# Optimization experiments

Hardware: AMD Instinct MI355X
Metric: run time of the kernel (lower is better)

The kernel has to match this reference:

```python
import jax, jax.numpy as jnp
import numpy as np

D_MODEL = 1024
STATE_DIM = 256


def setup_inputs() -> dict:
    key = jax.random.key(0)
    k_u, k_lam, k_B, k_C = jax.random.split(key, 4)
    u = jax.random.normal(k_u, (4, 4096, D_MODEL), dtype=jnp.float32)
    # log_lambda ~ N(3.0, 0.5^2), matching torch.randn(state_dim)*0.5 + 3.0
    log_lambda = jax.random.normal(k_lam, (STATE_DIM,), dtype=jnp.float32) * 0.5 + 3.0
    # torch Linear weights: B.weight [state_dim, d_model], C.weight [d_model, state_dim]
    B_w = jax.random.normal(k_B, (STATE_DIM, D_MODEL), dtype=jnp.float32) / np.sqrt(D_MODEL)
    C_w = jax.random.normal(k_C, (D_MODEL, STATE_DIM), dtype=jnp.float32) / np.sqrt(STATE_DIM)
    D = jnp.zeros((D_MODEL,), dtype=jnp.float32)
    return {"u": u, "log_lambda": log_lambda, "B_w": B_w, "C_w": C_w, "D": D}


def reference(u, log_lambda, B_w, C_w, D):
    # u: [batch, seq, d_model]
    lam = jax.nn.sigmoid(log_lambda)                      # [state_dim]
    Bu = jnp.einsum('bsd,nd->bsn', u, B_w)                # [batch, seq, state_dim]

    def step(h, bu_t):
        h = lam * h + bu_t                                # [batch, state_dim]
        return h, h

    h0 = jnp.zeros((u.shape[0], lam.shape[0]), dtype=u.dtype)
    # scan over time axis; Bu transposed to [seq, batch, state_dim]
    _, hs = jax.lax.scan(step, h0, jnp.swapaxes(Bu, 0, 1))
    hs = jnp.swapaxes(hs, 0, 1)                           # [batch, seq, state_dim]
    y = jnp.einsum('bsn,dn->bsd', hs, C_w) + D * u        # [batch, seq, d_model]
    return y
```

## Files before the change

kernel.cpp:

```cpp
#include <hip/hip_runtime.h>
#include <math.h>

typedef unsigned short ushort_t;
typedef __bf16 v8bf __attribute__((ext_vector_type(8)));
typedef float f32x4 __attribute__((ext_vector_type(4)));

#define BATCH 4
#define SEQ 4096
#define DM 1024
#define NS 256
#define MROWS (BATCH*SEQ)

#define NCH 128
#define CL (SEQ/NCH)

#define BM 128
#define BN 128
#define BK 32

typedef __attribute__((address_space(1))) void as1_void;
typedef __attribute__((address_space(3))) void as3_void;

__device__ __forceinline__ void gl_lds16(const void* g, void* l) {
    __builtin_amdgcn_global_load_lds((as1_void*)g, (as3_void*)l, 16, 0, 0);
}

__device__ __forceinline__ ushort_t f2bf(float f) {
    unsigned u = __builtin_bit_cast(unsigned, f);
    u += 0x7fff + ((u >> 16) & 1);
    return (ushort_t)(u >> 16);
}

__device__ __forceinline__ float sigm(float x) { return 1.0f / (1.0f + expf(-x)); }

template<bool FUSE_DU>
__global__ __launch_bounds__(256)
void gemm_bt_mfma(const ushort_t* __restrict__ A,
                  const ushort_t* __restrict__ B,
                  float* __restrict__ C,
                  int M, int N, int K,
                  const float* __restrict__ Dvec, const float* __restrict__ U)
{
    __shared__ __align__(16) ushort_t As[BM*BK];
    __shared__ __align__(16) ushort_t Bs[BN*BK];

    const int tid  = threadIdx.x;
    const int lane = tid & 63;
    const int wave = tid >> 6;
    const int wrow = wave >> 1;
    const int wcol = wave & 1;
    const int m0 = blockIdx.x * BM;
    const int n0 = blockIdx.y * BN;

    const int fr = lane & 15;
    const int fq = lane >> 4;

    f32x4 acc[4][4] = {};

    const int ch0 = wave*128 + lane;
    const int ch1 = ch0 + 64;

    for (int k0 = 0; k0 < K; k0 += BK) {
        __syncthreads();
        {
            int r0 = ch0 >> 2, c0 = (ch0 & 3) * 8;
            int r1 = ch1 >> 2, c1 = (ch1 & 3) * 8;
            gl_lds16(&A[(size_t)(m0 + r0)*K + k0 + c0], &As[ch0*8]);
            gl_lds16(&B[(size_t)(n0 + r0)*K + k0 + c0], &Bs[ch0*8]);
            gl_lds16(&A[(size_t)(m0 + r1)*K + k0 + c1], &As[ch1*8]);
            gl_lds16(&B[(size_t)(n0 + r1)*K + k0 + c1], &Bs[ch1*8]);
        }
        __syncthreads();

        v8bf af[4], bf[4];
        #pragma unroll
        for (int mi = 0; mi < 4; ++mi)
            af[mi] = *reinterpret_cast<const v8bf*>(&As[(wrow*64 + mi*16 + fr)*BK + fq*8]);
        #pragma unroll
        for (int ni = 0; ni < 4; ++ni)
            bf[ni] = *reinterpret_cast<const v8bf*>(&Bs[(wcol*64 + ni*16 + fr)*BK + fq*8]);

        #pragma unroll
        for (int mi = 0; mi < 4; ++mi)
            #pragma unroll
            for (int ni = 0; ni < 4; ++ni)
                acc[mi][ni] = __builtin_amdgcn_mfma_f32_16x16x32_bf16(
                                  af[mi], bf[ni], acc[mi][ni], 0, 0, 0);
    }

    const int orow = m0 + wrow*64 + (lane >> 4)*4;
    const int ocol = n0 + wcol*64 + (lane & 15);
    #pragma unroll
    for (int mi = 0; mi < 4; ++mi) {
        #pragma unroll
        for (int ni = 0; ni < 4; ++ni) {
            const int col = ocol + ni*16;
            #pragma unroll
            for (int r = 0; r < 4; ++r) {
                const size_t idx = (size_t)(orow + mi*16 + r) * N + col;
                float v = acc[mi][ni][r];
                if (FUSE_DU) v = fmaf(Dvec[col], U[idx], v);
                C[idx] = v;
            }
        }
    }
}

__global__ __launch_bounds__(256)
void cvt4(const float4* __restrict__ in, ushort_t* __restrict__ out, int n4)
{
    int i = blockIdx.x * 256 + threadIdx.x;
    if (i >= n4) return;
    float4 v = in[i];
    ushort4 o;
    o.x = f2bf(v.x); o.y = f2bf(v.y); o.z = f2bf(v.z); o.w = f2bf(v.w);
    *(ushort4*)&out[4*(size_t)i] = o;
}

__global__ __launch_bounds__(256)
void scan_finals(const float* __restrict__ Bu, const float* __restrict__ ll,
                 float* __restrict__ cf)
{
    const int n = threadIdx.x, c = blockIdx.x, b = blockIdx.y;
    const float lam = sigm(ll[n]);
    const size_t base = ((size_t)b*SEQ + (size_t)c*CL)*NS + n;
    float v[CL];
    #pragma unroll
    for (int t = 0; t < CL; ++t) v[t] = Bu[base + (size_t)t*NS];
    float h = 0.0f;
    #pragma unroll
    for (int t = 0; t < CL; ++t) h = fmaf(lam, h, v[t]);
    cf[((size_t)b*NCH + c)*NS + n] = h;
}

__global__ __launch_bounds__(256)
void carry_scan(const float* __restrict__ ll, const float* __restrict__ cf,
                float* __restrict__ carry)
{
    const int n = threadIdx.x, b = blockIdx.x;
    const float lam = sigm(ll[n]);
    float lamL = lam;
    #pragma unroll
    for (int i = 0; i < 5; ++i) lamL *= lamL;

    const float* cfb = cf    + (size_t)b*NCH*NS + n;
    float*       cab = carry + (size_t)b*NCH*NS + n;

    float x = 0.0f;
    for (int c0 = 0; c0 < NCH; c0 += 16) {
        float v[16];
        #pragma unroll
        for (int j = 0; j < 16; ++j) v[j] = cfb[(size_t)(c0 + j)*NS];
        #pragma unroll
        for (int j = 0; j < 16; ++j) {
            cab[(size_t)(c0 + j)*NS] = x;
            x = fmaf(lamL, x, v[j]);
        }
    }
}

__global__ __launch_bounds__(256)
void scan_apply(const float* __restrict__ Bu, const float* __restrict__ ll,
                const float* __restrict__ carry, ushort_t* __restrict__ hs16)
{
    const int n = threadIdx.x, c = blockIdx.x, b = blockIdx.y;
    const float lam = sigm(ll[n]);
    const size_t base = ((size_t)b*SEQ + (size_t)c*CL)*NS + n;

    float v[CL];
    #pragma unroll
    for (int t = 0; t < CL; ++t) v[t] = Bu[base + (size_t)t*NS];

    float h = carry[((size_t)b*NCH + c)*NS + n];
    #pragma unroll
    for (int t = 0; t < CL; ++t) { h = fmaf(lam, h, v[t]); v[t] = h; }
    #pragma unroll
    for (int t = 0; t < CL; ++t) hs16[base + (size_t)t*NS] = f2bf(v[t]);
}

extern "C" void kernel_launch(void* const* d_in, const int* in_sizes, int n_in,
                              void* d_out, int out_size, void* d_ws, size_t ws_size,
                              hipStream_t stream) {
    const float* u          = (const float*)d_in[0];
    const float* log_lambda = (const float*)d_in[1];
    const float* B_w        = (const float*)d_in[2];
    const float* C_w        = (const float*)d_in[3];
    const float* Dv         = (const float*)d_in[4];
    float* y  = (float*)d_out;

    char* w = (char*)d_ws;
    ushort_t* u16  = (ushort_t*)w;
    ushort_t* hs16 = (ushort_t*)w;
    float*    Bu   = (float*)(w + 33554432);
    ushort_t* Bw16 = (ushort_t*)(w + 33554432 + 16777216);
    ushort_t* Cw16 = (ushort_t*)(w + 33554432 + 16777216 + 524288);
    float*    cf   = (float*)(w + 33554432 + 16777216 + 1048576);
    float*    carry= (float*)(w + 33554432 + 16777216 + 1572864);

    dim3 blk(256);

    cvt4<<<dim3(MROWS*DM/4/256), blk, 0, stream>>>((const float4*)u,   u16,  MROWS*DM/4);
    cvt4<<<dim3(NS*DM/4/256),    blk, 0, stream>>>((const float4*)B_w, Bw16, NS*DM/4);
    cvt4<<<dim3(DM*NS/4/256),    blk, 0, stream>>>((const float4*)C_w, Cw16, DM*NS/4);

    gemm_bt_mfma<false><<<dim3(MROWS/BM, NS/BN), blk, 0, stream>>>(
        u16, Bw16, Bu, MROWS, NS, DM, nullptr, nullptr);

    scan_finals<<<dim3(NCH, BATCH), blk, 0, stream>>>(Bu, log_lambda, cf);
    carry_scan <<<dim3(BATCH),      blk, 0, stream>>>(log_lambda, cf, carry);
    scan_apply <<<dim3(NCH, BATCH), blk, 0, stream>>>(Bu, log_lambda, carry, hs16);

    gemm_bt_mfma<true><<<dim3(MROWS/BM, DM/BN), blk, 0, stream>>>(
        hs16, Cw16, y, MROWS, DM, NS, Dv, u);
}
```

Before: 187.3 us.

## Fuse input conversion and chunk-final scan into first GEMM, skip zero D

The first GEMM now reads fp32 u directly and converts it to bf16 while staging into LDS. This eliminates the separate conversion kernel and its bf16 buffer. Its epilogue also computes each 32-step chunk's final scan state using lambda-power weights and cross-lane shuffles, which replaces the scan_finals kernel. The weight conversions are merged into one launch, and the second GEMM skips reading u when the D coefficient is zero. The trade-offs are synchronous A loads in place of async LDS loads and extra epilogue math in GEMM1.

```diff
diff --git a/kernel.cpp b/kernel.cpp
--- a/kernel.cpp
+++ b/kernel.cpp
@@ -3,7 +3,9 @@
 
 typedef unsigned short ushort_t;
 typedef __bf16 v8bf __attribute__((ext_vector_type(8)));
-typedef float f32x4 __attribute__((ext_vector_type(4)));
+typedef __bf16 v4bf __attribute__((ext_vector_type(4)));
+typedef float  v4f  __attribute__((ext_vector_type(4)));
+typedef float  f32x4 __attribute__((ext_vector_type(4)));
 
 #define BATCH 4
 #define SEQ 4096
@@ -33,13 +35,139 @@
 
 __device__ __forceinline__ float sigm(float x) { return 1.0f / (1.0f + expf(-x)); }
 
-template<bool FUSE_DU>
-__global__ __launch_bounds__(256)
-void gemm_bt_mfma(const ushort_t* __restrict__ A,
-                  const ushort_t* __restrict__ B,
-                  float* __restrict__ C,
-                  int M, int N, int K,
-                  const float* __restrict__ Dvec, const float* __restrict__ U)
+__device__ __forceinline__ float powk(int e, float l1, float l2, float l4,
+                                      float l8, float l16) {
+    float w = 1.0f;
+    if (e & 1)  w *= l1;
+    if (e & 2)  w *= l2;
+    if (e & 4)  w *= l4;
+    if (e & 8)  w *= l8;
+    if (e & 16) w *= l16;
+    return w;
+}
+
+__global__ __launch_bounds__(256)
+void gemm1_fused(const float* __restrict__ A,
+                 const ushort_t* __restrict__ B,
+                 float* __restrict__ Bu,
+                 const float* __restrict__ ll,
+                 float* __restrict__ cf)
+{
+    const int K = DM;
+    const int N = NS;
+    __shared__ __align__(16) ushort_t As[BM*BK];
+    __shared__ __align__(16) ushort_t Bs[BN*BK];
+
+    const int tid  = threadIdx.x;
+    const int lane = tid & 63;
+    const int wave = tid >> 6;
+    const int wrow = wave >> 1;
+    const int wcol = wave & 1;
+    const int m0 = blockIdx.x * BM;
+    const int n0 = blockIdx.y * BN;
+
+    const int fr = lane & 15;
+    const int fq = lane >> 4;
+
+    f32x4 acc[4][4] = {};
+
+    const int bch0 = wave*128 + lane;
+    const int bch1 = bch0 + 64;
+
+    for (int k0 = 0; k0 < K; k0 += BK) {
+        __syncthreads();
+        {
+            int r0 = bch0 >> 2, c0 = (bch0 & 3) * 8;
+            int r1 = bch1 >> 2, c1 = (bch1 & 3) * 8;
+            gl_lds16(&B[(size_t)(n0 + r0)*K + k0 + c0], &Bs[bch0*8]);
+            gl_lds16(&B[(size_t)(n0 + r1)*K + k0 + c1], &Bs[bch1*8]);
+        }
+        {
+            v4f va[4];
+            #pragma unroll
+            for (int j = 0; j < 4; ++j) {
+                int cid = j*256 + tid;
+                int row = cid >> 3;
+                int c4  = (cid & 7) * 4;
+                va[j] = *(const v4f*)&A[(size_t)(m0 + row)*K + k0 + c4];
+            }
+            #pragma unroll
+            for (int j = 0; j < 4; ++j) {
+                int cid = j*256 + tid;
+                int row = cid >> 3;
+                int c4  = (cid & 7) * 4;
+                v4bf o = __builtin_convertvector(va[j], v4bf);
+                *(v4bf*)&As[row*BK + c4] = o;
+            }
+        }
+        __syncthreads();
+
+        v8bf af[4], bf[4];
+        #pragma unroll
+        for (int mi = 0; mi < 4; ++mi)
+            af[mi] = *reinterpret_cast<const v8bf*>(&As[(wrow*64 + mi*16 + fr)*BK + fq*8]);
+        #pragma unroll
+        for (int ni = 0; ni < 4; ++ni)
+            bf[ni] = *reinterpret_cast<const v8bf*>(&Bs[(wcol*64 + ni*16 + fr)*BK + fq*8]);
+
+        #pragma unroll
+        for (int mi = 0; mi < 4; ++mi)
+            #pragma unroll
+            for (int ni = 0; ni < 4; ++ni)
+                acc[mi][ni] = __builtin_amdgcn_mfma_f32_16x16x32_bf16(
+                                  af[mi], bf[ni], acc[mi][ni], 0, 0, 0);
+    }
+
+    const int orow = m0 + wrow*64 + (lane >> 4)*4;
+    const int ocol = n0 + wcol*64 + (lane & 15);
+    #pragma unroll
+    for (int mi = 0; mi < 4; ++mi)
+        #pragma unroll
+        for (int ni = 0; ni < 4; ++ni)
+            #pragma unroll
+            for (int r = 0; r < 4; ++r)
+                Bu[(size_t)(orow + mi*16 + r) * N + (ocol + ni*16)] = acc[mi][ni][r];
+
+    const int b_idx  = m0 >> 12;
+    const int c_base = (m0 & 4095) >> 5;
+    const int base   = (lane >> 4) * 4;
+
+    #pragma unroll
+    for (int ni = 0; ni < 4; ++ni) {
+        const int col = ocol + ni*16;
+        const float l1  = sigm(ll[col]);
+        const float l2  = l1*l1;
+        const float l4  = l2*l2;
+        const float l8  = l4*l4;
+        const float l16 = l8*l8;
+        #pragma unroll
+        for (int half = 0; half < 2; ++half) {
+            float f = 0.0f;
+            #pragma unroll
+            for (int mi2 = 0; mi2 < 2; ++mi2) {
+                const int mi = half*2 + mi2;
+                float w = powk(28 - mi2*16 - base, l1, l2, l4, l8, l16);
+                f = fmaf(w, acc[mi][ni][3], f);
+                w *= l1; f = fmaf(w, acc[mi][ni][2], f);
+                w *= l1; f = fmaf(w, acc[mi][ni][1], f);
+                w *= l1; f = fmaf(w, acc[mi][ni][0], f);
+            }
+            f += __shfl_xor(f, 16, 64);
+            f += __shfl_xor(f, 32, 64);
+            if ((lane >> 4) == 0) {
+                const int chunk = c_base + wrow*2 + half;
+                cf[((size_t)b_idx*NCH + chunk)*NS + col] = f;
+            }
+        }
+    }
+}
+
+__global__ __launch_bounds__(256)
+void gemm2_mfma(const ushort_t* __restrict__ A,
+                const ushort_t* __restrict__ B,
+                float* __restrict__ C,
+                int M, int N, int K,
+                const float* __restrict__ Dvec, const float* __restrict__ U)
 {
     __shared__ __align__(16) ushort_t As[BM*BK];
     __shared__ __align__(16) ushort_t Bs[BN*BK];
@@ -91,15 +219,16 @@
     const int orow = m0 + wrow*64 + (lane >> 4)*4;
     const int ocol = n0 + wcol*64 + (lane & 15);
     #pragma unroll
-    for (int mi = 0; mi < 4; ++mi) {
-        #pragma unroll
-        for (int ni = 0; ni < 4; ++ni) {
-            const int col = ocol + ni*16;
+    for (int ni = 0; ni < 4; ++ni) {
+        const int col = ocol + ni*16;
+        const float d = Dvec[col];
+        #pragma unroll
+        for (int mi = 0; mi < 4; ++mi) {
             #pragma unroll
             for (int r = 0; r < 4; ++r) {
                 const size_t idx = (size_t)(orow + mi*16 + r) * N + col;
                 float v = acc[mi][ni][r];
-                if (FUSE_DU) v = fmaf(Dvec[col], U[idx], v);
+                if (d != 0.0f) v = fmaf(d, U[idx], v);
                 C[idx] = v;
             }
         }
@@ -107,30 +236,16 @@
 }
 
 __global__ __launch_bounds__(256)
-void cvt4(const float4* __restrict__ in, ushort_t* __restrict__ out, int n4)
-{
-    int i = blockIdx.x * 256 + threadIdx.x;
-    if (i >= n4) return;
-    float4 v = in[i];
+void cvt_w(const float4* __restrict__ Bw, const float4* __restrict__ Cw,
+           ushort_t* __restrict__ Bo, ushort_t* __restrict__ Co)
+{
+    const int i = blockIdx.x * 256 + threadIdx.x;
+    const float4* src = blockIdx.y ? Cw : Bw;
+    ushort_t*     dst = blockIdx.y ? Co : Bo;
+    float4 v = src[i];
     ushort4 o;
     o.x = f2bf(v.x); o.y = f2bf(v.y); o.z = f2bf(v.z); o.w = f2bf(v.w);
-    *(ushort4*)&out[4*(size_t)i] = o;
-}
-
-__global__ __launch_bounds__(256)
-void scan_finals(const float* __restrict__ Bu, const float* __restrict__ ll,
-                 float* __restrict__ cf)
-{
-    const int n = threadIdx.x, c = blockIdx.x, b = blockIdx.y;
-    const float lam = sigm(ll[n]);
-    const size_t base = ((size_t)b*SEQ + (size_t)c*CL)*NS + n;
-    float v[CL];
-    #pragma unroll
-    for (int t = 0; t < CL; ++t) v[t] = Bu[base + (size_t)t*NS];
-    float h = 0.0f;
-    #pragma unroll
-    for (int t = 0; t < CL; ++t) h = fmaf(lam, h, v[t]);
-    cf[((size_t)b*NCH + c)*NS + n] = h;
+    *(ushort4*)&dst[4*(size_t)i] = o;
 }
 
 __global__ __launch_bounds__(256)
@@ -189,27 +304,24 @@
     float* y  = (float*)d_out;
 
     char* w = (char*)d_ws;
-    ushort_t* u16  = (ushort_t*)w;
-    ushort_t* hs16 = (ushort_t*)w;
-    float*    Bu   = (float*)(w + 33554432);
-    ushort_t* Bw16 = (ushort_t*)(w + 33554432 + 16777216);
-    ushort_t* Cw16 = (ushort_t*)(w + 33554432 + 16777216 + 524288);
-    float*    cf   = (float*)(w + 33554432 + 16777216 + 1048576);
-    float*    carry= (float*)(w + 33554432 + 16777216 + 1572864);
+    float*    Bu    = (float*)w;
+    ushort_t* hs16  = (ushort_t*)(w + 16777216);
+    ushort_t* Bw16  = (ushort_t*)(w + 25165824);
+    ushort_t* Cw16  = (ushort_t*)(w + 25690112);
+    float*    cf    = (float*)(w + 26214400);
+    float*    carry = (float*)(w + 26738688);
 
     dim3 blk(256);
 
-    cvt4<<<dim3(MROWS*DM/4/256), blk, 0, stream>>>((const float4*)u,   u16,  MROWS*DM/4);
-    cvt4<<<dim3(NS*DM/4/256),    blk, 0, stream>>>((const float4*)B_w, Bw16, NS*DM/4);
-    cvt4<<<dim3(DM*NS/4/256),    blk, 0, stream>>>((const float4*)C_w, Cw16, DM*NS/4);
-
-    gemm_bt_mfma<false><<<dim3(MROWS/BM, NS/BN), blk, 0, stream>>>(
-        u16, Bw16, Bu, MROWS, NS, DM, nullptr, nullptr);
-
-    scan_finals<<<dim3(NCH, BATCH), blk, 0, stream>>>(Bu, log_lambda, cf);
-    carry_scan <<<dim3(BATCH),      blk, 0, stream>>>(log_lambda, cf, carry);
-    scan_apply <<<dim3(NCH, BATCH), blk, 0, stream>>>(Bu, log_lambda, carry, hs16);
-
-    gemm_bt_mfma<true><<<dim3(MROWS/BM, DM/BN), blk, 0, stream>>>(
+    cvt_w<<<dim3(256, 2), blk, 0, stream>>>((const float4*)B_w, (const float4*)C_w,
+                                            Bw16, Cw16);
+
+    gemm1_fused<<<dim3(MROWS/BM, NS/BN), blk, 0, stream>>>(
+        u, Bw16, Bu, log_lambda, cf);
+
+    carry_scan<<<dim3(BATCH),      blk, 0, stream>>>(log_lambda, cf, carry);
+    scan_apply<<<dim3(NCH, BATCH), blk, 0, stream>>>(Bu, log_lambda, carry, hs16);
+
+    gemm2_mfma<<<dim3(MROWS/BM, DM/BN), blk, 0, stream>>>(
         hs16, Cw16, y, MROWS, DM, NS, Dv, u);
 }
```

Result: no change. 185.1 us (-1.1%).
